# Optimization experiments

Measured on AMD Instinct MI355X. Metric: run time of the kernel, lower is better.

The kernel has to match this reference:

```python
import jax, jax.numpy as jnp
import numpy as np

B, T, NG = 1024, 16, 23            # clips, window, nodes per timestep graph
H, IN, L, C = 64, 8, 20, 3         # hidden, input_dim, num_layers, classes
E_PER = 256                        # edges per graph
NUM_GRAPHS = B * T                 # 16384
N = NUM_GRAPHS * NG                # 376832 nodes
E = NUM_GRAPHS * E_PER             # 4194304 edges
LN_EPS = 1e-5


def setup_inputs() -> dict:
    key = jax.random.key(0)
    ks = jax.random.split(key, 16)
    s = 0.05
    x = jax.random.normal(ks[0], (N, IN), jnp.float32)
    # intra-graph random edges: global_id = graph_id * NG + local_id
    gid = jnp.repeat(jnp.arange(NUM_GRAPHS, dtype=jnp.int32), E_PER)
    src_l = jax.random.randint(ks[1], (E,), 0, NG, dtype=jnp.int32)
    dst_l = jax.random.randint(ks[2], (E,), 0, NG, dtype=jnp.int32)
    edge_index = jnp.stack([gid * NG + src_l, gid * NG + dst_l])
    batch = jnp.repeat(jnp.arange(NUM_GRAPHS, dtype=jnp.int32), NG)
    return {
        "x": x,
        "edge_index": edge_index,
        "batch": batch,
        "W_enc": jax.random.normal(ks[3], (IN, H), jnp.float32) * s,
        "b_enc": jnp.zeros((H,), jnp.float32),
        "ln_g": jnp.ones((L, H), jnp.float32),
        "ln_b": jnp.zeros((L, H), jnp.float32),
        "W_rel": jax.random.normal(ks[4], (L, H, H), jnp.float32) * s,
        "b_rel": jnp.zeros((L, H), jnp.float32),
        "W_root": jax.random.normal(ks[5], (L, H, H), jnp.float32) * s,
        "pos": jax.random.normal(ks[6], (1, T, H), jnp.float32) * 0.02,
        "W1": jax.random.normal(ks[7], (H, H), jnp.float32) * s,
        "b1": jnp.zeros((H,), jnp.float32),
        "W2": jax.random.normal(ks[8], (H, C), jnp.float32) * s,
        "b2": jnp.zeros((C,), jnp.float32),
    }


def _layer_norm(h, g, b):
    mu = jnp.mean(h, axis=-1, keepdims=True)
    var = jnp.mean(jnp.square(h - mu), axis=-1, keepdims=True)
    return (h - mu) * jax.lax.rsqrt(var + LN_EPS) * g + b


def reference(x, edge_index, batch, W_enc, b_enc, ln_g, ln_b, W_rel, b_rel,
              W_root, pos, W1, b1, W2, b2):
    src, dst = edge_index[0], edge_index[1]
    h = x @ W_enc + b_enc                      # node encoder, [N, H]

    # DeepGCNLayer block='res+': out = x + GraphConv(relu(LN(x)))
    # GraphConv: lin_rel(sum_{j->i} z_j) + lin_root(z)  (aggr='add')
    def step(h, p):
        g, b, Wr, br, Wo = p
        z = jax.nn.relu(_layer_norm(h, g, b))  # dropout = identity (eval)
        agg = jax.ops.segment_sum(z[src], dst, num_segments=N)
        return h + agg @ Wr + br + z @ Wo, None

    h, _ = jax.lax.scan(step, h, (ln_g, ln_b, W_rel, b_rel, W_root))

    # global mean pool (each graph has exactly NG nodes)
    pooled = jax.ops.segment_sum(h, batch, num_segments=NUM_GRAPHS) / NG
    xt = pooled.reshape(B, T, H) + pos[:, :T, :]
    v = jnp.mean(xt, axis=1)                   # temporal 'pool'
    h1 = jax.nn.relu(v @ W1 + b1)
    return h1 @ W2 + b2                        # [B, C]
```

## Files before the change

kernel.cpp:

```cpp
#include <hip/hip_runtime.h>
#include <hip/hip_bf16.h>

#define NGRAPH 16384
#define NG     23
#define HD     64
#define INF    8
#define LAYERS 20
#define EDGES_PER 256
#define E_TOT  (NGRAPH * EDGES_PER)
#define BATCH  1024
#define TWIN   16
#define CLS    3

#define NS 48

typedef __attribute__((ext_vector_type(8))) short s8v;
typedef __attribute__((ext_vector_type(4))) float f4v;
typedef __attribute__((ext_vector_type(2))) float f2v;

union FragU { unsigned u[4]; s8v v; };

__device__ inline f2v vlo(f4v v) { return (f2v){v[0], v[1]}; }
__device__ inline f2v vhi(f4v v) { return (f2v){v[2], v[3]}; }

__device__ inline unsigned pk2_bf16(f2v v) {
  __hip_bfloat162 b = __float22bfloat162_rn(make_float2(v[0], v[1]));
  unsigned r;
  __builtin_memcpy(&r, &b, sizeof(r));
  return r;
}

__device__ inline f2v max0(f2v v) {
#if defined(__has_builtin) && __has_builtin(__builtin_elementwise_max)
  return __builtin_elementwise_max(v, (f2v){0.f, 0.f});
#else
  return (f2v){fmaxf(v[0], 0.f), fmaxf(v[1], 0.f)};
#endif
}

__device__ inline unsigned f2bf_pk(float a, float b) {
  unsigned ua = __builtin_bit_cast(unsigned, a);
  unsigned ub = __builtin_bit_cast(unsigned, b);
  ua = ua + 0x7FFFu + ((ua >> 16) & 1u);
  ub = ub + 0x7FFFu + ((ub >> 16) & 1u);
  return (ua >> 16) | (ub & 0xFFFF0000u);
}

__global__ __launch_bounds__(256) void build_adj(const int* __restrict__ ei,
                                                 unsigned* __restrict__ adjf) {
  __shared__ int cnt[4][NG * NG];
  const int grp = threadIdx.x >> 6, lane = threadIdx.x & 63;
  const int g = blockIdx.x * 4 + grp;
  for (int i = lane; i < NG * NG; i += 64) cnt[grp][i] = 0;
  __syncthreads();
  const int base = g * EDGES_PER, goff = g * NG;
#pragma unroll
  for (int r = 0; r < EDGES_PER / 64; ++r) {
    const int e = base + r * 64 + lane;
    atomicAdd(&cnt[grp][(ei[E_TOT + e] - goff) * NG + (ei[e] - goff)], 1);
  }
  __syncthreads();
  const int col = lane & 15, quad = lane >> 4;
#pragma unroll
  for (int Nt = 0; Nt < 2; ++Nt) {
    const int dst = col + 16 * Nt;
    unsigned pk[4];
#pragma unroll
    for (int w = 0; w < 4; ++w) {
      const int s0 = quad * 8 + 2 * w, s1 = s0 + 1;
      float v0 = 0.f, v1 = 0.f;
      if (dst < NG) {
        if (s0 < NG) v0 = (float)cnt[grp][dst * NG + s0];
        if (s1 < NG) v1 = (float)cnt[grp][dst * NG + s1];
      }
      pk[w] = f2bf_pk(v0, v1);
    }
    uint4 q; q.x = pk[0]; q.y = pk[1]; q.z = pk[2]; q.w = pk[3];
    *(uint4*)&adjf[(((size_t)g * 2 + Nt) * 64 + lane) * 4] = q;
  }
}

__global__ __launch_bounds__(256) void pack_w(const float* __restrict__ W_rel,
                                              const float* __restrict__ W_root,
                                              unsigned* __restrict__ wf) {
  const int tid = blockIdx.x * 256 + threadIdx.x;
  if (tid >= LAYERS * 2 * 4 * 2 * 64) return;
  const int lane = tid & 63, fi = tid >> 6;
  const int Kt = fi & 1, Mt = (fi >> 1) & 3, m = (fi >> 3) & 1, l = fi >> 4;
  const float* W = (m ? W_root : W_rel) + (size_t)l * HD * HD;
  const int col = lane & 15, quad = lane >> 4;
  const int jdim = Mt * 16 + col;
  unsigned pk[4];
#pragma unroll
  for (int w = 0; w < 4; ++w) {
    const int j0 = 2 * w, j1 = 2 * w + 1;
    const int d0 = ((j0 >> 2) * 2 + Kt) * 16 + quad * 4 + (j0 & 3);
    const int d1 = ((j1 >> 2) * 2 + Kt) * 16 + quad * 4 + (j1 & 3);
    pk[w] = f2bf_pk(W[(size_t)d0 * HD + jdim], W[(size_t)d1 * HD + jdim]);
  }
  uint4 q; q.x = pk[0]; q.y = pk[1]; q.z = pk[2]; q.w = pk[3];
  *(uint4*)&wf[(size_t)tid * 4] = q;
}

__global__ __launch_bounds__(256) void gcn_main(
    const float* __restrict__ x, const unsigned* __restrict__ adjf,
    const unsigned* __restrict__ wf,
    const float* __restrict__ W_enc, const float* __restrict__ b_enc,
    const float* __restrict__ ln_g, const float* __restrict__ ln_b,
    const float* __restrict__ b_rel, float* __restrict__ pooled) {
  __shared__ __align__(16) unsigned short sm[4 * HD * NS];
  const int lane = threadIdx.x & 63, wv = threadIdx.x >> 6;
  const int g = blockIdx.x * 4 + wv;
  const int col = lane & 15, quad = lane >> 4;
  unsigned short* zt = sm + wv * (HD * NS);

  const s8v adjB0 = *(const s8v*)&adjf[(((size_t)g * 2 + 0) * 64 + lane) * 4];
  const s8v adjB1 = *(const s8v*)&adjf[(((size_t)g * 2 + 1) * 64 + lane) * 4];

  const int nsw[2] = { col ^ (quad << 3), (col + 16) ^ (quad << 3) };

  f4v acc[4][2];
  {
    f4v xa[2][2];
    const f4v zz = {0.f, 0.f, 0.f, 0.f};
#pragma unroll
    for (int Nt = 0; Nt < 2; ++Nt) {
      const int n = col + 16 * Nt;
      if (n < NG) {
        const float* xp = x + ((size_t)g * NG + n) * INF;
        xa[Nt][0] = *(const f4v*)xp;
        xa[Nt][1] = *(const f4v*)(xp + 4);
      } else { xa[Nt][0] = zz; xa[Nt][1] = zz; }
    }
#pragma unroll
    for (int Mt = 0; Mt < 4; ++Mt) {
      const f4v be = *(const f4v*)(b_enc + Mt * 16 + quad * 4);
      acc[Mt][0] = be; acc[Mt][1] = be;
#pragma unroll
      for (int i = 0; i < INF; ++i) {
        const f4v we = *(const f4v*)(W_enc + i * HD + Mt * 16 + quad * 4);
        acc[Mt][0] += we * xa[0][i >> 2][i & 3];
        acc[Mt][1] += we * xa[1][i >> 2][i & 3];
      }
    }
  }

#pragma unroll 1
  for (int l = 0; l < LAYERS; ++l) {
    const unsigned* wbase = wf + (size_t)l * (2 * 4 * 2 * 64 * 4);
    f4v gf[4], bfv[4];
#pragma unroll
    for (int Mt = 0; Mt < 4; ++Mt) {
      gf[Mt]  = *(const f4v*)(ln_g + l * HD + Mt * 16 + quad * 4);
      bfv[Mt] = *(const f4v*)(ln_b + l * HD + Mt * 16 + quad * 4);
    }

    float mu[2], rs[2];
    {
      float sh[2], qh[2];
#pragma unroll
      for (int Nt = 0; Nt < 2; ++Nt) {
        f2v t = vlo(acc[0][Nt]) + vhi(acc[0][Nt]);
        t += vlo(acc[1][Nt]); t += vhi(acc[1][Nt]);
        t += vlo(acc[2][Nt]); t += vhi(acc[2][Nt]);
        t += vlo(acc[3][Nt]); t += vhi(acc[3][Nt]);
        f2v u = vlo(acc[0][Nt]) * vlo(acc[0][Nt]);
        u += vhi(acc[0][Nt]) * vhi(acc[0][Nt]);
        u += vlo(acc[1][Nt]) * vlo(acc[1][Nt]);
        u += vhi(acc[1][Nt]) * vhi(acc[1][Nt]);
        u += vlo(acc[2][Nt]) * vlo(acc[2][Nt]);
        u += vhi(acc[2][Nt]) * vhi(acc[2][Nt]);
        u += vlo(acc[3][Nt]) * vlo(acc[3][Nt]);
        u += vhi(acc[3][Nt]) * vhi(acc[3][Nt]);
        sh[Nt] = t[0] + t[1];
        qh[Nt] = u[0] + u[1];
      }
      sh[0] += __shfl_xor(sh[0], 16); sh[1] += __shfl_xor(sh[1], 16);
      qh[0] += __shfl_xor(qh[0], 16); qh[1] += __shfl_xor(qh[1], 16);
      sh[0] += __shfl_xor(sh[0], 32); sh[1] += __shfl_xor(sh[1], 32);
      qh[0] += __shfl_xor(qh[0], 32); qh[1] += __shfl_xor(qh[1], 32);
#pragma unroll
      for (int Nt = 0; Nt < 2; ++Nt) {
        mu[Nt] = sh[Nt] * (1.0f / HD);
        float var = fmaf(qh[Nt], (1.0f / HD), -mu[Nt] * mu[Nt]);
        var = fmaxf(var, 0.f);
        rs[Nt] = rsqrtf(var + 1e-5f);
      }
    }

    FragU zpk[2][2];
#pragma unroll
    for (int Kt = 0; Kt < 2; ++Kt) {
#pragma unroll
      for (int hi = 0; hi < 2; ++hi) {
        const int Mt = Kt + 2 * hi;
        const f2v gl = vlo(gf[Mt]), gh = vhi(gf[Mt]);
        const f2v bl = vlo(bfv[Mt]), bh = vhi(bfv[Mt]);
#pragma unroll
        for (int Nt = 0; Nt < 2; ++Nt) {
          const f2v sgl = gl * rs[Nt], sgh = gh * rs[Nt];
          const f2v tbl = bl - mu[Nt] * sgl, tbh = bh - mu[Nt] * sgh;
          const f2v zl = max0(vlo(acc[Mt][Nt]) * sgl + tbl);
          const f2v zh = max0(vhi(acc[Mt][Nt]) * sgh + tbh);
          zpk[Kt][Nt].u[hi * 2 + 0] = pk2_bf16(zl);
          zpk[Kt][Nt].u[hi * 2 + 1] = pk2_bf16(zh);
        }
      }
#pragma unroll
      for (int hi = 0; hi < 2; ++hi) {
        const int Mt = Kt + 2 * hi;
        const int dbase = Mt * 16 + quad * 4;
#pragma unroll
        for (int Nt = 0; Nt < 2; ++Nt)
#pragma unroll
          for (int r2 = 0; r2 < 2; ++r2) {
            const unsigned d = zpk[Kt][Nt].u[hi * 2 + r2];
            zt[(dbase + 2 * r2    ) * NS + nsw[Nt]] = (unsigned short)d;
            zt[(dbase + 2 * r2 + 1) * NS + nsw[Nt]] = (unsigned short)(d >> 16);
          }
      }
    }

#pragma unroll
    for (int Kt = 0; Kt < 2; ++Kt)
#pragma unroll
      for (int Mt = 0; Mt < 4; ++Mt) {
        const s8v wo = *(const s8v*)&wbase[((((1 * 4) + Mt) * 2 + Kt) * 64 + lane) * 4];
#pragma unroll
        for (int Nt = 0; Nt < 2; ++Nt)
          acc[Mt][Nt] = __builtin_amdgcn_mfma_f32_16x16x32_bf16(wo, zpk[Kt][Nt].v, acc[Mt][Nt], 0, 0, 0);
      }

    asm volatile("s_waitcnt lgkmcnt(0)" ::: "memory");

    FragU za[4];
#pragma unroll
    for (int Mt = 0; Mt < 4; ++Mt) {
      const int dim = Mt * 16 + col;
      const int qq = (quad ^ (col >> 2)) * 8;
      za[Mt].v = *(const s8v*)&zt[dim * NS + qq];
    }

    const f4v zzero = {0.f, 0.f, 0.f, 0.f};
    f4v ag[4][2];
#pragma unroll
    for (int Mt = 0; Mt < 4; ++Mt) {
      ag[Mt][0] = __builtin_amdgcn_mfma_f32_16x16x32_bf16(za[Mt].v, adjB0, zzero, 0, 0, 0);
      ag[Mt][1] = __builtin_amdgcn_mfma_f32_16x16x32_bf16(za[Mt].v, adjB1, zzero, 0, 0, 0);
    }

#pragma unroll
    for (int Kt = 0; Kt < 2; ++Kt) {
      FragU apk[2];
#pragma unroll
      for (int Nt = 0; Nt < 2; ++Nt) {
        apk[Nt].u[0] = pk2_bf16(vlo(ag[Kt    ][Nt]));
        apk[Nt].u[1] = pk2_bf16(vhi(ag[Kt    ][Nt]));
        apk[Nt].u[2] = pk2_bf16(vlo(ag[Kt + 2][Nt]));
        apk[Nt].u[3] = pk2_bf16(vhi(ag[Kt + 2][Nt]));
      }
#pragma unroll
      for (int Mt = 0; Mt < 4; ++Mt) {
        const s8v wr = *(const s8v*)&wbase[((((0 * 4) + Mt) * 2 + Kt) * 64 + lane) * 4];
#pragma unroll
        for (int Nt = 0; Nt < 2; ++Nt)
          acc[Mt][Nt] = __builtin_amdgcn_mfma_f32_16x16x32_bf16(wr, apk[Nt].v, acc[Mt][Nt], 0, 0, 0);
      }
    }

#pragma unroll
    for (int Mt = 0; Mt < 4; ++Mt) {
      const f4v brf = *(const f4v*)(b_rel + l * HD + Mt * 16 + quad * 4);
      const f2v bl = vlo(brf), bh = vhi(brf);
#pragma unroll
      for (int Nt = 0; Nt < 2; ++Nt) {
        const f2v al = vlo(acc[Mt][Nt]) + bl;
        const f2v ah = vhi(acc[Mt][Nt]) + bh;
        acc[Mt][Nt] = (f4v){al[0], al[1], ah[0], ah[1]};
      }
    }
  }

  float* hb = (float*)zt;
  asm volatile("s_waitcnt lgkmcnt(0)" ::: "memory");
#pragma unroll
  for (int Mt = 0; Mt < 4; ++Mt)
#pragma unroll
    for (int Nt = 0; Nt < 2; ++Nt) {
      const int n = col + 16 * Nt;
      if (n < NG) *(f4v*)&hb[n * HD + Mt * 16 + quad * 4] = acc[Mt][Nt];
    }
  asm volatile("s_waitcnt lgkmcnt(0)" ::: "memory");
  float s = 0.f;
#pragma unroll
  for (int n = 0; n < NG; ++n) s += hb[n * HD + lane];
  pooled[(size_t)g * HD + lane] = s;
}

__global__ __launch_bounds__(64) void head(
    const float* __restrict__ pooled, const float* __restrict__ pos,
    const float* __restrict__ W1, const float* __restrict__ b1,
    const float* __restrict__ W2, const float* __restrict__ b2,
    float* __restrict__ out) {
  __shared__ float sv[HD];
  __shared__ float sh1[HD];
  const int b = blockIdx.x, k = threadIdx.x;
  float v = 0.f;
#pragma unroll
  for (int tt = 0; tt < TWIN; ++tt) v += pooled[((size_t)(b * TWIN + tt)) * HD + k];
  float p = 0.f;
#pragma unroll
  for (int tt = 0; tt < TWIN; ++tt) p += pos[tt * HD + k];
  v = v * (1.0f / (NG * TWIN)) + p * (1.0f / TWIN);
  sv[k] = v;
  __syncthreads();
  float a = b1[k];
#pragma unroll
  for (int kk = 0; kk < HD; ++kk) a = fmaf(sv[kk], W1[kk * HD + k], a);
  a = fmaxf(a, 0.f);
  sh1[k] = a;
  __syncthreads();
  if (k < CLS) {
    float o = b2[k];
#pragma unroll
    for (int kk = 0; kk < HD; ++kk) o = fmaf(sh1[kk], W2[kk * CLS + k], o);
    out[(size_t)b * CLS + k] = o;
  }
}

extern "C" void kernel_launch(void* const* d_in, const int* in_sizes, int n_in,
                              void* d_out, int out_size, void* d_ws, size_t ws_size,
                              hipStream_t stream) {
  const float* x      = (const float*)d_in[0];
  const int*   ei     = (const int*)  d_in[1];
  const float* W_enc  = (const float*)d_in[3];
  const float* b_enc  = (const float*)d_in[4];
  const float* ln_g   = (const float*)d_in[5];
  const float* ln_b   = (const float*)d_in[6];
  const float* W_rel  = (const float*)d_in[7];
  const float* b_rel  = (const float*)d_in[8];
  const float* W_root = (const float*)d_in[9];
  const float* pos    = (const float*)d_in[10];
  const float* W1     = (const float*)d_in[11];
  const float* b1     = (const float*)d_in[12];
  const float* W2     = (const float*)d_in[13];
  const float* b2     = (const float*)d_in[14];
  float* out = (float*)d_out;

  char* p = (char*)d_ws;
  unsigned* wfrag   = (unsigned*)p;  p += (size_t)LAYERS * 2 * 4 * 2 * 64 * 16;
  unsigned* adjfrag = (unsigned*)p;  p += (size_t)NGRAPH * 2 * 64 * 16;
  float*    pooled  = (float*)p;

  pack_w   <<<80, 256, 0, stream>>>(W_rel, W_root, wfrag);
  build_adj<<<NGRAPH / 4, 256, 0, stream>>>(ei, adjfrag);
  gcn_main <<<NGRAPH / 4, 256, 0, stream>>>(x, adjfrag, wfrag, W_enc, b_enc,
                                            ln_g, ln_b, b_rel, pooled);
  head     <<<BATCH, 64, 0, stream>>>(pooled, pos, W1, b1, W2, b2, out);
}
```

Measured before the change: 464.2 us.

## Pack two graphs per wavefront and fuse adjacency build into main kernel

Each wavefront now handles a pair of graphs (46 node columns across three 16-wide tiles) rather than one graph padded from 23 to 32 columns. This cuts MFMA padding waste, since 48 padded columns now cover 46 real ones instead of 32 covering 23. The separate build_adj kernel and its global adjacency buffer are removed. Each wave builds packed 16-bit edge counts in LDS and turns them into bf16 adjacency fragments in registers. The cost is more register pressure (acc[4][3], adjB[3][2]), a larger LDS tile (NS 64), and a pooling epilogue that has to split the outputs of the two graphs.

```diff
diff --git a/kernel.cpp b/kernel.cpp
--- a/kernel.cpp
+++ b/kernel.cpp
@@ -2,7 +2,9 @@
 #include <hip/hip_bf16.h>
 
 #define NGRAPH 16384
+#define NPAIR  (NGRAPH / 2)
 #define NG     23
+#define PCOLS  46
 #define HD     64
 #define INF    8
 #define LAYERS 20
@@ -12,7 +14,7 @@
 #define TWIN   16
 #define CLS    3
 
-#define NS 48
+#define NS 64
 
 typedef __attribute__((ext_vector_type(8))) short s8v;
 typedef __attribute__((ext_vector_type(4))) float f4v;
@@ -44,40 +46,6 @@
   ua = ua + 0x7FFFu + ((ua >> 16) & 1u);
   ub = ub + 0x7FFFu + ((ub >> 16) & 1u);
   return (ua >> 16) | (ub & 0xFFFF0000u);
-}
-
-__global__ __launch_bounds__(256) void build_adj(const int* __restrict__ ei,
-                                                 unsigned* __restrict__ adjf) {
-  __shared__ int cnt[4][NG * NG];
-  const int grp = threadIdx.x >> 6, lane = threadIdx.x & 63;
-  const int g = blockIdx.x * 4 + grp;
-  for (int i = lane; i < NG * NG; i += 64) cnt[grp][i] = 0;
-  __syncthreads();
-  const int base = g * EDGES_PER, goff = g * NG;
-#pragma unroll
-  for (int r = 0; r < EDGES_PER / 64; ++r) {
-    const int e = base + r * 64 + lane;
-    atomicAdd(&cnt[grp][(ei[E_TOT + e] - goff) * NG + (ei[e] - goff)], 1);
-  }
-  __syncthreads();
-  const int col = lane & 15, quad = lane >> 4;
-#pragma unroll
-  for (int Nt = 0; Nt < 2; ++Nt) {
-    const int dst = col + 16 * Nt;
-    unsigned pk[4];
-#pragma unroll
-    for (int w = 0; w < 4; ++w) {
-      const int s0 = quad * 8 + 2 * w, s1 = s0 + 1;
-      float v0 = 0.f, v1 = 0.f;
-      if (dst < NG) {
-        if (s0 < NG) v0 = (float)cnt[grp][dst * NG + s0];
-        if (s1 < NG) v1 = (float)cnt[grp][dst * NG + s1];
-      }
-      pk[w] = f2bf_pk(v0, v1);
-    }
-    uint4 q; q.x = pk[0]; q.y = pk[1]; q.z = pk[2]; q.w = pk[3];
-    *(uint4*)&adjf[(((size_t)g * 2 + Nt) * 64 + lane) * 4] = q;
-  }
 }
 
 __global__ __launch_bounds__(256) void pack_w(const float* __restrict__ W_rel,
@@ -103,31 +71,89 @@
 }
 
 __global__ __launch_bounds__(256) void gcn_main(
-    const float* __restrict__ x, const unsigned* __restrict__ adjf,
+    const float* __restrict__ x, const int* __restrict__ ei,
     const unsigned* __restrict__ wf,
     const float* __restrict__ W_enc, const float* __restrict__ b_enc,
     const float* __restrict__ ln_g, const float* __restrict__ ln_b,
     const float* __restrict__ b_rel, float* __restrict__ pooled) {
   __shared__ __align__(16) unsigned short sm[4 * HD * NS];
   const int lane = threadIdx.x & 63, wv = threadIdx.x >> 6;
-  const int g = blockIdx.x * 4 + wv;
+  const int p = blockIdx.x * 4 + wv;
   const int col = lane & 15, quad = lane >> 4;
   unsigned short* zt = sm + wv * (HD * NS);
 
-  const s8v adjB0 = *(const s8v*)&adjf[(((size_t)g * 2 + 0) * 64 + lane) * 4];
-  const s8v adjB1 = *(const s8v*)&adjf[(((size_t)g * 2 + 1) * 64 + lane) * 4];
-
-  const int nsw[2] = { col ^ (quad << 3), (col + 16) ^ (quad << 3) };
-
-  f4v acc[4][2];
+  unsigned* cnt = (unsigned*)zt;
+  for (int i = lane; i < 48 * 24; i += 64) cnt[i] = 0;
+  asm volatile("s_waitcnt lgkmcnt(0)" ::: "memory");
   {
-    f4v xa[2][2];
+    const int ebase = p * (2 * EDGES_PER);
+    const int noff = p * PCOLS;
+#pragma unroll
+    for (int r = 0; r < 8; ++r) {
+      const int e = ebase + r * 64 + lane;
+      const int s = ei[e] - noff;
+      const int d = ei[E_TOT + e] - noff;
+      atomicAdd(&cnt[d * 24 + (s >> 1)], 1u << ((s & 1) * 16));
+    }
+  }
+  asm volatile("s_waitcnt lgkmcnt(0)" ::: "memory");
+
+  FragU adjB[3][2];
+#pragma unroll
+  for (int Nt = 0; Nt < 3; ++Nt) {
+    const int dst = col + 16 * Nt;
+    const bool dok = dst < PCOLS;
+#pragma unroll
+    for (int Kt = 0; Kt < 2; ++Kt)
+#pragma unroll
+      for (int w = 0; w < 4; ++w) {
+        const int s0 = Kt * 32 + quad * 8 + 2 * w;
+        float v0 = 0.f, v1 = 0.f;
+        if (dok && s0 < PCOLS) {
+          const unsigned rd = cnt[dst * 24 + (s0 >> 1)];
+          v0 = (float)(rd & 0xffffu);
+          if (s0 + 1 < PCOLS) v1 = (float)(rd >> 16);
+        }
+        adjB[Nt][Kt].u[w] = f2bf_pk(v0, v1);
+      }
+  }
+  asm volatile("s_waitcnt lgkmcnt(0)" ::: "memory");
+
+  {
+    uint4 z4; z4.x = 0; z4.y = 0; z4.z = 0; z4.w = 0;
+    for (int i = lane; i < (HD * NS * 2) / 16; i += 64) ((uint4*)zt)[i] = z4;
+  }
+  asm volatile("s_waitcnt lgkmcnt(0)" ::: "memory");
+
+  int wb[3][4];
+#pragma unroll
+  for (int Nt = 0; Nt < 3; ++Nt) {
+    const int node = col + 16 * Nt;
+#pragma unroll
+    for (int dd = 0; dd < 4; ++dd) {
+      const int d = quad * 4 + dd;
+      wb[Nt][dd] = d * NS + ((((node >> 3) ^ ((d >> 1) & 7))) << 3) + (node & 7);
+    }
+  }
+  int ra[4][2];
+#pragma unroll
+  for (int Mt = 0; Mt < 4; ++Mt) {
+    const int dim = Mt * 16 + col;
+#pragma unroll
+    for (int Kt = 0; Kt < 2; ++Kt)
+      ra[Mt][Kt] = dim * NS + (((Kt * 4 + quad) ^ ((dim >> 1) & 7)) << 3);
+  }
+
+  f4v acc[4][3];
+  {
+    const float* xg = x + (size_t)p * PCOLS * INF;
+    f4v xa[3][2];
     const f4v zz = {0.f, 0.f, 0.f, 0.f};
 #pragma unroll
-    for (int Nt = 0; Nt < 2; ++Nt) {
-      const int n = col + 16 * Nt;
-      if (n < NG) {
-        const float* xp = x + ((size_t)g * NG + n) * INF;
+    for (int Nt = 0; Nt < 3; ++Nt) {
+      const int c = col + 16 * Nt;
+      if (c < PCOLS) {
+        const float* xp = xg + (size_t)c * INF;
         xa[Nt][0] = *(const f4v*)xp;
         xa[Nt][1] = *(const f4v*)(xp + 4);
       } else { xa[Nt][0] = zz; xa[Nt][1] = zz; }
@@ -135,12 +161,13 @@
 #pragma unroll
     for (int Mt = 0; Mt < 4; ++Mt) {
       const f4v be = *(const f4v*)(b_enc + Mt * 16 + quad * 4);
-      acc[Mt][0] = be; acc[Mt][1] = be;
+      acc[Mt][0] = be; acc[Mt][1] = be; acc[Mt][2] = be;
 #pragma unroll
       for (int i = 0; i < INF; ++i) {
         const f4v we = *(const f4v*)(W_enc + i * HD + Mt * 16 + quad * 4);
         acc[Mt][0] += we * xa[0][i >> 2][i & 3];
         acc[Mt][1] += we * xa[1][i >> 2][i & 3];
+        acc[Mt][2] += we * xa[2][i >> 2][i & 3];
       }
     }
   }
@@ -155,11 +182,11 @@
       bfv[Mt] = *(const f4v*)(ln_b + l * HD + Mt * 16 + quad * 4);
     }
 
-    float mu[2], rs[2];
+    float mu[3], rs[3];
     {
-      float sh[2], qh[2];
-#pragma unroll
-      for (int Nt = 0; Nt < 2; ++Nt) {
+      float sh[3], qh[3];
+#pragma unroll
+      for (int Nt = 0; Nt < 3; ++Nt) {
         f2v t = vlo(acc[0][Nt]) + vhi(acc[0][Nt]);
         t += vlo(acc[1][Nt]); t += vhi(acc[1][Nt]);
         t += vlo(acc[2][Nt]); t += vhi(acc[2][Nt]);
@@ -175,12 +202,12 @@
         sh[Nt] = t[0] + t[1];
         qh[Nt] = u[0] + u[1];
       }
-      sh[0] += __shfl_xor(sh[0], 16); sh[1] += __shfl_xor(sh[1], 16);
-      qh[0] += __shfl_xor(qh[0], 16); qh[1] += __shfl_xor(qh[1], 16);
-      sh[0] += __shfl_xor(sh[0], 32); sh[1] += __shfl_xor(sh[1], 32);
-      qh[0] += __shfl_xor(qh[0], 32); qh[1] += __shfl_xor(qh[1], 32);
-#pragma unroll
-      for (int Nt = 0; Nt < 2; ++Nt) {
+#pragma unroll
+      for (int Nt = 0; Nt < 3; ++Nt) { sh[Nt] += __shfl_xor(sh[Nt], 16); qh[Nt] += __shfl_xor(qh[Nt], 16); }
+#pragma unroll
+      for (int Nt = 0; Nt < 3; ++Nt) { sh[Nt] += __shfl_xor(sh[Nt], 32); qh[Nt] += __shfl_xor(qh[Nt], 32); }
+#pragma unroll
+      for (int Nt = 0; Nt < 3; ++Nt) {
         mu[Nt] = sh[Nt] * (1.0f / HD);
         float var = fmaf(qh[Nt], (1.0f / HD), -mu[Nt] * mu[Nt]);
         var = fmaxf(var, 0.f);
@@ -188,7 +215,7 @@
       }
     }
 
-    FragU zpk[2][2];
+    FragU zpk[2][3];
 #pragma unroll
     for (int Kt = 0; Kt < 2; ++Kt) {
 #pragma unroll
@@ -197,7 +224,7 @@
         const f2v gl = vlo(gf[Mt]), gh = vhi(gf[Mt]);
         const f2v bl = vlo(bfv[Mt]), bh = vhi(bfv[Mt]);
 #pragma unroll
-        for (int Nt = 0; Nt < 2; ++Nt) {
+        for (int Nt = 0; Nt < 3; ++Nt) {
           const f2v sgl = gl * rs[Nt], sgh = gh * rs[Nt];
           const f2v tbl = bl - mu[Nt] * sgl, tbh = bh - mu[Nt] * sgh;
           const f2v zl = max0(vlo(acc[Mt][Nt]) * sgl + tbl);
@@ -209,14 +236,13 @@
 #pragma unroll
       for (int hi = 0; hi < 2; ++hi) {
         const int Mt = Kt + 2 * hi;
-        const int dbase = Mt * 16 + quad * 4;
-#pragma unroll
-        for (int Nt = 0; Nt < 2; ++Nt)
+#pragma unroll
+        for (int Nt = 0; Nt < 3; ++Nt)
 #pragma unroll
           for (int r2 = 0; r2 < 2; ++r2) {
             const unsigned d = zpk[Kt][Nt].u[hi * 2 + r2];
-            zt[(dbase + 2 * r2    ) * NS + nsw[Nt]] = (unsigned short)d;
-            zt[(dbase + 2 * r2 + 1) * NS + nsw[Nt]] = (unsigned short)(d >> 16);
+            zt[Mt * (16 * NS) + wb[Nt][2 * r2    ]] = (unsigned short)d;
+            zt[Mt * (16 * NS) + wb[Nt][2 * r2 + 1]] = (unsigned short)(d >> 16);
           }
       }
     }
@@ -227,33 +253,30 @@
       for (int Mt = 0; Mt < 4; ++Mt) {
         const s8v wo = *(const s8v*)&wbase[((((1 * 4) + Mt) * 2 + Kt) * 64 + lane) * 4];
 #pragma unroll
-        for (int Nt = 0; Nt < 2; ++Nt)
+        for (int Nt = 0; Nt < 3; ++Nt)
           acc[Mt][Nt] = __builtin_amdgcn_mfma_f32_16x16x32_bf16(wo, zpk[Kt][Nt].v, acc[Mt][Nt], 0, 0, 0);
       }
 
     asm volatile("s_waitcnt lgkmcnt(0)" ::: "memory");
 
-    FragU za[4];
+    const f4v zzero = {0.f, 0.f, 0.f, 0.f};
+    f4v ag[4][3];
 #pragma unroll
     for (int Mt = 0; Mt < 4; ++Mt) {
-      const int dim = Mt * 16 + col;
-      const int qq = (quad ^ (col >> 2)) * 8;
-      za[Mt].v = *(const s8v*)&zt[dim * NS + qq];
-    }
-
-    const f4v zzero = {0.f, 0.f, 0.f, 0.f};
-    f4v ag[4][2];
-#pragma unroll
-    for (int Mt = 0; Mt < 4; ++Mt) {
-      ag[Mt][0] = __builtin_amdgcn_mfma_f32_16x16x32_bf16(za[Mt].v, adjB0, zzero, 0, 0, 0);
-      ag[Mt][1] = __builtin_amdgcn_mfma_f32_16x16x32_bf16(za[Mt].v, adjB1, zzero, 0, 0, 0);
+      const s8v za0 = *(const s8v*)&zt[ra[Mt][0]];
+      const s8v za1 = *(const s8v*)&zt[ra[Mt][1]];
+#pragma unroll
+      for (int Nt = 0; Nt < 3; ++Nt) {
+        ag[Mt][Nt] = __builtin_amdgcn_mfma_f32_16x16x32_bf16(za0, adjB[Nt][0].v, zzero, 0, 0, 0);
+        ag[Mt][Nt] = __builtin_amdgcn_mfma_f32_16x16x32_bf16(za1, adjB[Nt][1].v, ag[Mt][Nt], 0, 0, 0);
+      }
     }
 
 #pragma unroll
     for (int Kt = 0; Kt < 2; ++Kt) {
-      FragU apk[2];
-#pragma unroll
-      for (int Nt = 0; Nt < 2; ++Nt) {
+      FragU apk[3];
+#pragma unroll
+      for (int Nt = 0; Nt < 3; ++Nt) {
         apk[Nt].u[0] = pk2_bf16(vlo(ag[Kt    ][Nt]));
         apk[Nt].u[1] = pk2_bf16(vhi(ag[Kt    ][Nt]));
         apk[Nt].u[2] = pk2_bf16(vlo(ag[Kt + 2][Nt]));
@@ -263,7 +286,7 @@
       for (int Mt = 0; Mt < 4; ++Mt) {
         const s8v wr = *(const s8v*)&wbase[((((0 * 4) + Mt) * 2 + Kt) * 64 + lane) * 4];
 #pragma unroll
-        for (int Nt = 0; Nt < 2; ++Nt)
+        for (int Nt = 0; Nt < 3; ++Nt)
           acc[Mt][Nt] = __builtin_amdgcn_mfma_f32_16x16x32_bf16(wr, apk[Nt].v, acc[Mt][Nt], 0, 0, 0);
       }
     }
@@ -273,7 +296,7 @@
       const f4v brf = *(const f4v*)(b_rel + l * HD + Mt * 16 + quad * 4);
       const f2v bl = vlo(brf), bh = vhi(brf);
 #pragma unroll
-      for (int Nt = 0; Nt < 2; ++Nt) {
+      for (int Nt = 0; Nt < 3; ++Nt) {
         const f2v al = vlo(acc[Mt][Nt]) + bl;
         const f2v ah = vhi(acc[Mt][Nt]) + bh;
         acc[Mt][Nt] = (f4v){al[0], al[1], ah[0], ah[1]};
@@ -286,15 +309,23 @@
 #pragma unroll
   for (int Mt = 0; Mt < 4; ++Mt)
 #pragma unroll
-    for (int Nt = 0; Nt < 2; ++Nt) {
-      const int n = col + 16 * Nt;
-      if (n < NG) *(f4v*)&hb[n * HD + Mt * 16 + quad * 4] = acc[Mt][Nt];
-    }
-  asm volatile("s_waitcnt lgkmcnt(0)" ::: "memory");
-  float s = 0.f;
-#pragma unroll
-  for (int n = 0; n < NG; ++n) s += hb[n * HD + lane];
-  pooled[(size_t)g * HD + lane] = s;
+    for (int Nt = 0; Nt < 2; ++Nt)
+      *(f4v*)&hb[(col + 16 * Nt) * HD + Mt * 16 + quad * 4] = acc[Mt][Nt];
+  asm volatile("s_waitcnt lgkmcnt(0)" ::: "memory");
+  float sA = 0.f, sB = 0.f;
+#pragma unroll
+  for (int c = 0; c < NG; ++c) sA += hb[c * HD + lane];
+#pragma unroll
+  for (int c = NG; c < 32; ++c) sB += hb[c * HD + lane];
+  asm volatile("s_waitcnt lgkmcnt(0)" ::: "memory");
+#pragma unroll
+  for (int Mt = 0; Mt < 4; ++Mt)
+    *(f4v*)&hb[col * HD + Mt * 16 + quad * 4] = acc[Mt][2];
+  asm volatile("s_waitcnt lgkmcnt(0)" ::: "memory");
+#pragma unroll
+  for (int c = 0; c < PCOLS - 32; ++c) sB += hb[c * HD + lane];
+  pooled[(size_t)(2 * p) * HD + lane] = sA;
+  pooled[(size_t)(2 * p + 1) * HD + lane] = sB;
 }
 
 __global__ __launch_bounds__(64) void head(
@@ -348,13 +379,11 @@
   float* out = (float*)d_out;
 
   char* p = (char*)d_ws;
-  unsigned* wfrag   = (unsigned*)p;  p += (size_t)LAYERS * 2 * 4 * 2 * 64 * 16;
-  unsigned* adjfrag = (unsigned*)p;  p += (size_t)NGRAPH * 2 * 64 * 16;
-  float*    pooled  = (float*)p;
-
-  pack_w   <<<80, 256, 0, stream>>>(W_rel, W_root, wfrag);
-  build_adj<<<NGRAPH / 4, 256, 0, stream>>>(ei, adjfrag);
-  gcn_main <<<NGRAPH / 4, 256, 0, stream>>>(x, adjfrag, wfrag, W_enc, b_enc,
-                                            ln_g, ln_b, b_rel, pooled);
-  head     <<<BATCH, 64, 0, stream>>>(pooled, pos, W1, b1, W2, b2, out);
-}
+  unsigned* wfrag  = (unsigned*)p;  p += (size_t)LAYERS * 2 * 4 * 2 * 64 * 16;
+  float*    pooled = (float*)p;
+
+  pack_w  <<<80, 256, 0, stream>>>(W_rel, W_root, wfrag);
+  gcn_main<<<NPAIR / 4, 256, 0, stream>>>(x, ei, wfrag, W_enc, b_enc,
+                                          ln_g, ln_b, b_rel, pooled);
+  head    <<<BATCH, 64, 0, stream>>>(pooled, pos, W1, b1, W2, b2, out);
+}
```

Result: slower. 485.7 us (+4.6%).
